# Kernel optimization log

Hardware: AMD Instinct MI355X
Metric: run time of the kernel (lower is better)

The kernel has to match this reference:

```python
import jax, jax.numpy as jnp
import numpy as np

N, M, D = 8192, 8192, 64

def setup_inputs() -> dict:
    key = jax.random.key(0)
    kx, ky = jax.random.split(key)
    x = jax.random.normal(kx, (N, D), dtype=jnp.float32)
    y = jax.random.normal(ky, (M, D), dtype=jnp.float32)
    return {"x": x, "y": y}

def reference(x, y):
    T = 1.0
    # Dmat = 2 - euclidean cdist(x, y), computed via the Gram trick.
    sq = (jnp.sum(x * x, axis=1)[:, None]
          + jnp.sum(y * y, axis=1)[None, :]
          - 2.0 * (x @ y.T))
    Dmat = 2.0 - jnp.sqrt(jnp.maximum(sq, 0.0))          # [N, M]
    logprob_rows = jax.nn.log_softmax(Dmat * T, axis=1)   # [N, M]
    logprob_cols = jax.nn.log_softmax(Dmat.T * T, axis=1) # [M, N]
    choice_rows = jnp.argmax(logprob_rows, axis=1)        # [N]
    choice_cols = jnp.argmax(logprob_cols, axis=1)        # [M]
    seq = jnp.arange(M, dtype=choice_cols.dtype)
    mutual = choice_rows[choice_cols] == seq              # [M] bool
    lp_rows = jnp.take_along_axis(logprob_rows, choice_rows[:, None], axis=1)[:, 0]  # [N]
    lp_cols = jnp.take_along_axis(logprob_cols, choice_cols[:, None], axis=1)[:, 0]  # [M]
    # Padded (jit-friendly) form of the boolean compaction: entries where
    # mutual is False are zeroed; mutual mask identifies valid matches.
    log_probs = jnp.where(mutual, lp_rows[choice_cols] + lp_cols, 0.0)  # [M]
    dmatches = jnp.stack([choice_cols, seq], axis=1)      # [M, 2]
    return (log_probs, dmatches, mutual)
```

## Files before the change

### kernel.cpp

```cpp
#include <hip/hip_runtime.h>
#include <stdint.h>

#define NROWS 8192
#define MCOLS 8192
#define DDIM  64

typedef _Float16 half8   __attribute__((ext_vector_type(8)));
typedef float    floatx4 __attribute__((ext_vector_type(4)));

__device__ __forceinline__ unsigned f2key(float f) {
  unsigned u = __float_as_uint(f);
  return (u & 0x80000000u) ? ~u : (u | 0x80000000u);
}
__device__ __forceinline__ float key2f(unsigned k) {
  unsigned u = (k & 0x80000000u) ? (k & 0x7fffffffu) : ~k;
  return __uint_as_float(u);
}

__global__ void convert_kernel(const float* __restrict__ x, const float* __restrict__ y,
                               _Float16* __restrict__ xh, _Float16* __restrict__ xl,
                               _Float16* __restrict__ yh, _Float16* __restrict__ yl,
                               float* __restrict__ xn, float* __restrict__ yn,
                               unsigned long long* __restrict__ rk,
                               unsigned long long* __restrict__ ck,
                               float* __restrict__ rs, float* __restrict__ cs) {
  __shared__ float lnorm[32];
  const int gid = blockIdx.x * 256 + threadIdx.x;
  if (gid < 8192) { rk[gid] = 0ull; rs[gid] = 0.0f; ck[gid] = 0ull; cs[gid] = 0.0f; }
  if (threadIdx.x < 32) lnorm[threadIdx.x] = 0.0f;
  __syncthreads();

  const float* src; _Float16 *dh, *dl; float* nout; int t, rowbase;
  if (gid < 65536) { src = x; dh = xh; dl = xl; nout = xn; t = gid;
                     rowbase = blockIdx.x * 32; }
  else             { src = y; dh = yh; dl = yl; nout = yn; t = gid - 65536;
                     rowbase = (blockIdx.x - 256) * 32; }

  const int lane = t & 63;
  const int c    = (t >> 6) & 1;
  const int p    = t >> 7;
  const int row  = p * 16 + (lane & 15);
  const int k0   = c * 32 + ((lane >> 4) << 3);
  const float* s = src + (size_t)row * DDIM + k0;

  float fb[8];
  *(floatx4*)(&fb[0]) = *(const floatx4*)(s);
  *(floatx4*)(&fb[4]) = *(const floatx4*)(s + 4);

  _Float16 hbuf[8], lbuf[8];
  float s8 = 0.0f;
  #pragma unroll
  for (int j = 0; j < 8; ++j) {
    float f = fb[j];
    _Float16 h = (_Float16)f;
    hbuf[j] = h;
    lbuf[j] = (_Float16)((f - (float)h) * 2048.0f);
    s8 = fmaf(f, f, s8);
  }
  size_t o = (size_t)t * 8;
  *(half8*)(dh + o) = *(half8*)hbuf;
  *(half8*)(dl + o) = *(half8*)lbuf;

  atomicAdd(&lnorm[((p & 1) << 4) | (t & 15)], s8);
  __syncthreads();
  if (threadIdx.x < 32) nout[rowbase + threadIdx.x] = lnorm[threadIdx.x];
}

#define MFMA16(A, B, C) __builtin_amdgcn_mfma_f32_16x16x32_f16((A), (B), (C), 0, 0, 0)

__global__ __launch_bounds__(256, 3) void mfma_tile_kernel(
    const _Float16* __restrict__ xh, const _Float16* __restrict__ xl,
    const _Float16* __restrict__ yh, const _Float16* __restrict__ yl,
    const float* __restrict__ xn, const float* __restrict__ yn,
    unsigned long long* __restrict__ row_key, float* __restrict__ row_sum,
    unsigned long long* __restrict__ col_key, float* __restrict__ col_sum)
{
  __shared__ unsigned long long lkey[256];
  __shared__ float              lsum[256];

  const int wave = threadIdx.x >> 6;
  const int lane = threadIdx.x & 63;
  const int l15  = lane & 15;
  const int g    = lane >> 4;
  const int ap0  = blockIdx.y * 8 + wave * 2;
  const int ro   = ap0 * 16 + g * 4;
  const int colbase = blockIdx.x * 256;

  lkey[threadIdx.x] = 0ull;
  lsum[threadIdx.x] = 0.0f;
  __syncthreads();

  const half8* xh8 = (const half8*)xh;
  const half8* xl8 = (const half8*)xl;
  const half8* yh8 = (const half8*)yh;
  const half8* yl8 = (const half8*)yl;
  const size_t a0 = (size_t)ap0 * 128 + lane;
  half8 Ah[2][2], Al[2][2];
  #pragma unroll
  for (int p = 0; p < 2; ++p) {
    Ah[p][0] = xh8[a0 + p * 128];      Ah[p][1] = xh8[a0 + p * 128 + 64];
    Al[p][0] = xl8[a0 + p * 128];      Al[p][1] = xl8[a0 + p * 128 + 64];
  }

  float xne[8], rsum[8], rmax[8]; int ridx[8];
  #pragma unroll
  for (int s = 0; s < 8; ++s) {
    xne[s]  = xn[ro + ((s >> 2) << 4) + (s & 3)];
    rsum[s] = 0.0f; rmax[s] = -3.4e38f; ridx[s] = 0;
  }

  const size_t bcol0 = (size_t)(blockIdx.x * 16) * 128 + lane;

  half8 b0h0, b0h1, b0l0, b0l1; float y0n;
  half8 b1h0, b1h1, b1l0, b1l1; float y1n;
  b0h0 = yh8[bcol0];        b0h1 = yh8[bcol0 + 64];
  b0l0 = yl8[bcol0];        b0l1 = yl8[bcol0 + 64];
  y0n  = yn[colbase + l15];
  b1h0 = yh8[bcol0 + 128];  b1h1 = yh8[bcol0 + 192];
  b1l0 = yl8[bcol0 + 128];  b1l1 = yl8[bcol0 + 192];
  y1n  = yn[colbase + 16 + l15];

#define MFMA_TILE(BH0, BH1, BL0, BL1, O1A, O2A, O1B, O2B)                      \
  {                                                                            \
    floatx4 c1_ = {}, c2_ = {};                                                \
    c1_ = MFMA16(Ah[0][0], BH0, c1_);                                          \
    c1_ = MFMA16(Ah[0][1], BH1, c1_);                                          \
    c2_ = MFMA16(Al[0][0], BH0, c2_);                                          \
    c2_ = MFMA16(Al[0][1], BH1, c2_);                                          \
    c2_ = MFMA16(Ah[0][0], BL0, c2_);                                          \
    c2_ = MFMA16(Ah[0][1], BL1, c2_);                                          \
    O1A = c1_; O2A = c2_;                                                      \
    floatx4 d1_ = {}, d2_ = {};                                                \
    d1_ = MFMA16(Ah[1][0], BH0, d1_);                                          \
    d1_ = MFMA16(Ah[1][1], BH1, d1_);                                          \
    d2_ = MFMA16(Al[1][0], BH0, d2_);                                          \
    d2_ = MFMA16(Al[1][1], BH1, d2_);                                          \
    d2_ = MFMA16(Ah[1][0], BL0, d2_);                                          \
    d2_ = MFMA16(Ah[1][1], BL1, d2_);                                          \
    O1B = d1_; O2B = d2_;                                                      \
  }

#define EPILOGUE(JT, C1A, C2A, C1B, C2B, YNC)                                  \
  {                                                                            \
    const int col_ = colbase + (JT) * 16 + l15;                                \
    float cmax_ = -3.4e38f; int cidx_ = 0;                                     \
    float epan0_, epan1_;                                                      \
    {                                                                          \
      float ee_[4];                                                            \
      _Pragma("unroll")                                                        \
      for (int r = 0; r < 4; ++r) {                                            \
        const int s_ = r;                                                      \
        float dot = fmaf(C2A[r], (1.0f / 2048.0f), C1A[r]);                    \
        float sq  = fmaxf(fmaf(-2.0f, dot, xne[s_] + (YNC)), 0.0f);            \
        float d   = 2.0f - __builtin_amdgcn_sqrtf(sq);                         \
        float e   = __expf(d);                                                 \
        rsum[s_] += e;                                                         \
        if (d > rmax[s_]) ridx[s_] = col_;       \
        rmax[s_] = fmaxf(rmax[s_], d);                                         \
        if (d > cmax_) cidx_ = s_;               \
        cmax_ = fmaxf(cmax_, d);                                               \
        ee_[r] = e;                                                            \
      }                                                                        \
      epan0_ = (ee_[0] + ee_[1]) + (ee_[2] + ee_[3]);                          \
    }                                                                          \
    {                                                                          \
      float ee_[4];                                                            \
      _Pragma("unroll")                                                        \
      for (int r = 0; r < 4; ++r) {                                            \
        const int s_ = 4 + r;                                                  \
        float dot = fmaf(C2B[r], (1.0f / 2048.0f), C1B[r]);                    \
        float sq  = fmaxf(fmaf(-2.0f, dot, xne[s_] + (YNC)), 0.0f);            \
        float d   = 2.0f - __builtin_amdgcn_sqrtf(sq);                         \
        float e   = __expf(d);                                                 \
        rsum[s_] += e;                                                         \
        if (d > rmax[s_]) ridx[s_] = col_;                                     \
        rmax[s_] = fmaxf(rmax[s_], d);                                         \
        if (d > cmax_) cidx_ = s_;                                             \
        cmax_ = fmaxf(cmax_, d);                                               \
        ee_[r] = e;                                                            \
      }                                                                        \
      epan1_ = (ee_[0] + ee_[1]) + (ee_[2] + ee_[3]);                          \
    }                                                                          \
    float csum_ = epan0_ + epan1_;                \
    int crow_ = ro + ((cidx_ >> 2) << 4) + (cidx_ & 3);                        \
    unsigned long long ckey_ =                                                 \
        ((unsigned long long)f2key(cmax_) << 32) |                             \
        (unsigned long long)(unsigned)(~(unsigned)crow_);                      \
    atomicMax(&lkey[(JT) * 16 + l15], ckey_);                  \
    atomicAdd(&lsum[(JT) * 16 + l15], csum_);                  \
  }

  floatx4 Pc1a, Pc2a, Pc1b, Pc2b;
  floatx4 Qc1a, Qc2a, Qc1b, Qc2b;

  MFMA_TILE(b0h0, b0h1, b0l0, b0l1, Pc1a, Pc2a, Pc1b, Pc2b);

  for (int jt = 0; jt < 14; jt += 2) {
    {
      float ycur = y0n;
      const size_t bn = bcol0 + (size_t)(jt + 2) * 128;
      b0h0 = yh8[bn];      b0h1 = yh8[bn + 64];
      b0l0 = yl8[bn];      b0l1 = yl8[bn + 64];
      y0n  = yn[colbase + (jt + 2) * 16 + l15];
      MFMA_TILE(b1h0, b1h1, b1l0, b1l1, Qc1a, Qc2a, Qc1b, Qc2b);
      EPILOGUE(jt, Pc1a, Pc2a, Pc1b, Pc2b, ycur);
    }
    {
      float ycur = y1n;
      const size_t bn = bcol0 + (size_t)(jt + 3) * 128;
      b1h0 = yh8[bn];      b1h1 = yh8[bn + 64];
      b1l0 = yl8[bn];      b1l1 = yl8[bn + 64];
      y1n  = yn[colbase + (jt + 3) * 16 + l15];
      MFMA_TILE(b0h0, b0h1, b0l0, b0l1, Pc1a, Pc2a, Pc1b, Pc2b);
      EPILOGUE(jt + 1, Qc1a, Qc2a, Qc1b, Qc2b, ycur);
    }
  }
  {
    MFMA_TILE(b1h0, b1h1, b1l0, b1l1, Qc1a, Qc2a, Qc1b, Qc2b);
    EPILOGUE(14, Pc1a, Pc2a, Pc1b, Pc2b, y0n);
  }
  EPILOGUE(15, Qc1a, Qc2a, Qc1b, Qc2b, y1n);

#undef MFMA_TILE
#undef EPILOGUE

  unsigned long long rkk[8];
  #pragma unroll
  for (int s = 0; s < 8; ++s)
    rkk[s] = ((unsigned long long)f2key(rmax[s]) << 32) |
             (unsigned long long)(unsigned)(~(unsigned)ridx[s]);
  #pragma unroll
  for (int off = 1; off < 16; off <<= 1) {
    #pragma unroll
    for (int s = 0; s < 8; ++s) {
      rsum[s] += __shfl_xor(rsum[s], off);
      unsigned long long o = __shfl_xor(rkk[s], off);
      if (o > rkk[s]) rkk[s] = o;
    }
  }
  if (l15 == 0) {
    #pragma unroll
    for (int s = 0; s < 8; ++s) {
      int row = ro + ((s >> 2) << 4) + (s & 3);
      atomicMax(row_key + row, rkk[s]);
      atomicAdd(row_sum + row, rsum[s]);
    }
  }

  __syncthreads();
  {
    int col = colbase + threadIdx.x;
    atomicMax(col_key + col, lkey[threadIdx.x]);
    atomicAdd(col_sum + col, lsum[threadIdx.x]);
  }
}

__global__ void finalize_kernel(const unsigned long long* __restrict__ row_key,
                                const float* __restrict__ row_sum,
                                const unsigned long long* __restrict__ col_key,
                                const float* __restrict__ col_sum,
                                float* __restrict__ out)
{
  int j = blockIdx.x * 256 + threadIdx.x;
  if (j >= MCOLS) return;
  unsigned long long ck = col_key[j];
  int   ci   = (int)(~(unsigned)ck);
  float cmax = key2f((unsigned)(ck >> 32));
  float lp_col = cmax - logf(col_sum[j]);

  unsigned long long rk = row_key[ci];
  int   rj   = (int)(~(unsigned)rk);
  float rmax = key2f((unsigned)(rk >> 32));
  float lp_row = rmax - logf(row_sum[ci]);

  int mut = (rj == j);
  out[j]                 = mut ? (lp_row + lp_col) : 0.0f;
  out[MCOLS + 2 * j + 0] = (float)ci;
  out[MCOLS + 2 * j + 1] = (float)j;
  out[3 * MCOLS + j]     = mut ? 1.0f : 0.0f;
}

extern "C" void kernel_launch(void* const* d_in, const int* in_sizes, int n_in,
                              void* d_out, int out_size, void* d_ws, size_t ws_size,
                              hipStream_t stream) {
  const float* x = (const float*)d_in[0];
  const float* y = (const float*)d_in[1];
  float* out = (float*)d_out;

  char* ws = (char*)d_ws;
  unsigned long long* row_key = (unsigned long long*)(ws);
  unsigned long long* col_key = (unsigned long long*)(ws + 65536);
  float* row_sum = (float*)(ws + 131072);
  float* col_sum = (float*)(ws + 163840);
  float* xn      = (float*)(ws + 196608);
  float* yn      = (float*)(ws + 229376);
  _Float16* xh = (_Float16*)(ws + 262144);
  _Float16* xl = (_Float16*)(ws + 262144 + 1048576);
  _Float16* yh = (_Float16*)(ws + 262144 + 2097152);
  _Float16* yl = (_Float16*)(ws + 262144 + 3145728);

  convert_kernel<<<512, 256, 0, stream>>>(x, y, xh, xl, yh, yl, xn, yn,
                                          row_key, col_key, row_sum, col_sum);
  dim3 grid(MCOLS / 256, NROWS / 128);
  mfma_tile_kernel<<<grid, 256, 0, stream>>>(xh, xl, yh, yl, xn, yn,
                                             row_key, row_sum, col_key, col_sum);
  finalize_kernel<<<32, 256, 0, stream>>>(row_key, row_sum, col_key, col_sum, out);
}
```

Baseline: 123.8 us.

## Replace global atomics with per-block partial buffers and separate reductions

The tile kernel stores per-block row and column max-key and sum partials into workspace arrays instead of issuing global atomicMax/atomicAdd. A new row-reduction kernel combines the 32 column-block partials per row, and the finalize kernel reduces the 64 row-block partials per column. This is meant to remove atomic contention and the zero-initialisation in the convert kernel. In exchange it adds extra memory traffic for the partial arrays and an additional kernel launch.

After: 128.7 us. 4.0% more time.

```diff
diff --git a/kernel.cpp b/kernel.cpp
--- a/kernel.cpp
+++ b/kernel.cpp
@@ -4,6 +4,8 @@
 #define NROWS 8192
 #define MCOLS 8192
 #define DDIM  64
+#define NBX   32
+#define NBY   64
 
 typedef _Float16 half8   __attribute__((ext_vector_type(8)));
 typedef float    floatx4 __attribute__((ext_vector_type(4)));
@@ -20,13 +22,9 @@
 __global__ void convert_kernel(const float* __restrict__ x, const float* __restrict__ y,
                                _Float16* __restrict__ xh, _Float16* __restrict__ xl,
                                _Float16* __restrict__ yh, _Float16* __restrict__ yl,
-                               float* __restrict__ xn, float* __restrict__ yn,
-                               unsigned long long* __restrict__ rk,
-                               unsigned long long* __restrict__ ck,
-                               float* __restrict__ rs, float* __restrict__ cs) {
+                               float* __restrict__ xn, float* __restrict__ yn) {
   __shared__ float lnorm[32];
   const int gid = blockIdx.x * 256 + threadIdx.x;
-  if (gid < 8192) { rk[gid] = 0ull; rs[gid] = 0.0f; ck[gid] = 0ull; cs[gid] = 0.0f; }
   if (threadIdx.x < 32) lnorm[threadIdx.x] = 0.0f;
   __syncthreads();
 
@@ -72,8 +70,8 @@
     const _Float16* __restrict__ xh, const _Float16* __restrict__ xl,
     const _Float16* __restrict__ yh, const _Float16* __restrict__ yl,
     const float* __restrict__ xn, const float* __restrict__ yn,
-    unsigned long long* __restrict__ row_key, float* __restrict__ row_sum,
-    unsigned long long* __restrict__ col_key, float* __restrict__ col_sum)
+    unsigned long long* __restrict__ row_part_key, float* __restrict__ row_part_sum,
+    unsigned long long* __restrict__ col_part_key, float* __restrict__ col_part_sum)
 {
   __shared__ unsigned long long lkey[256];
   __shared__ float              lsum[256];
@@ -242,31 +240,57 @@
     #pragma unroll
     for (int s = 0; s < 8; ++s) {
       int row = ro + ((s >> 2) << 4) + (s & 3);
-      atomicMax(row_key + row, rkk[s]);
-      atomicAdd(row_sum + row, rsum[s]);
+      row_part_key[(size_t)blockIdx.x * NROWS + row] = rkk[s];
+      row_part_sum[(size_t)blockIdx.x * NROWS + row] = rsum[s];
     }
   }
 
   __syncthreads();
   {
     int col = colbase + threadIdx.x;
-    atomicMax(col_key + col, lkey[threadIdx.x]);
-    atomicAdd(col_sum + col, lsum[threadIdx.x]);
-  }
+    col_part_key[(size_t)blockIdx.y * MCOLS + col] = lkey[threadIdx.x];
+    col_part_sum[(size_t)blockIdx.y * MCOLS + col] = lsum[threadIdx.x];
+  }
+}
+
+__global__ void reduce_rows_kernel(const unsigned long long* __restrict__ rpk,
+                                   const float* __restrict__ rps,
+                                   unsigned long long* __restrict__ row_key,
+                                   float* __restrict__ row_sum)
+{
+  int row = blockIdx.x * 256 + threadIdx.x;
+  if (row >= NROWS) return;
+  unsigned long long best = 0ull; float sum = 0.0f;
+  #pragma unroll 8
+  for (int bx = 0; bx < NBX; ++bx) {
+    unsigned long long k = rpk[(size_t)bx * NROWS + row];
+    if (k > best) best = k;
+    sum += rps[(size_t)bx * NROWS + row];
+  }
+  row_key[row] = best;
+  row_sum[row] = sum;
 }
 
 __global__ void finalize_kernel(const unsigned long long* __restrict__ row_key,
                                 const float* __restrict__ row_sum,
-                                const unsigned long long* __restrict__ col_key,
-                                const float* __restrict__ col_sum,
+                                const unsigned long long* __restrict__ cpk,
+                                const float* __restrict__ cps,
                                 float* __restrict__ out)
 {
   int j = blockIdx.x * 256 + threadIdx.x;
   if (j >= MCOLS) return;
-  unsigned long long ck = col_key[j];
+
+  unsigned long long ck = 0ull; float csum = 0.0f;
+  #pragma unroll 8
+  for (int by = 0; by < NBY; ++by) {
+    unsigned long long k = cpk[(size_t)by * MCOLS + j];
+    if (k > ck) ck = k;
+    csum += cps[(size_t)by * MCOLS + j];
+  }
+
   int   ci   = (int)(~(unsigned)ck);
   float cmax = key2f((unsigned)(ck >> 32));
-  float lp_col = cmax - logf(col_sum[j]);
+  float lp_col = cmax - logf(csum);
 
   unsigned long long rk = row_key[ci];
   int   rj   = (int)(~(unsigned)rk);
@@ -289,20 +313,22 @@
 
   char* ws = (char*)d_ws;
   unsigned long long* row_key = (unsigned long long*)(ws);
-  unsigned long long* col_key = (unsigned long long*)(ws + 65536);
-  float* row_sum = (float*)(ws + 131072);
-  float* col_sum = (float*)(ws + 163840);
-  float* xn      = (float*)(ws + 196608);
-  float* yn      = (float*)(ws + 229376);
-  _Float16* xh = (_Float16*)(ws + 262144);
-  _Float16* xl = (_Float16*)(ws + 262144 + 1048576);
-  _Float16* yh = (_Float16*)(ws + 262144 + 2097152);
-  _Float16* yl = (_Float16*)(ws + 262144 + 3145728);
-
-  convert_kernel<<<512, 256, 0, stream>>>(x, y, xh, xl, yh, yl, xn, yn,
-                                          row_key, col_key, row_sum, col_sum);
+  float* row_sum = (float*)(ws + 65536);
+  float* xn      = (float*)(ws + 98304);
+  float* yn      = (float*)(ws + 131072);
+  unsigned long long* rpk = (unsigned long long*)(ws + 163840);
+  float* rps     = (float*)(ws + 2260992);
+  unsigned long long* cpk = (unsigned long long*)(ws + 3309568);
+  float* cps     = (float*)(ws + 7503872);
+  _Float16* xh = (_Float16*)(ws + 9601024);
+  _Float16* xl = (_Float16*)(ws + 10649600);
+  _Float16* yh = (_Float16*)(ws + 11698176);
+  _Float16* yl = (_Float16*)(ws + 12746752);
+
+  convert_kernel<<<512, 256, 0, stream>>>(x, y, xh, xl, yh, yl, xn, yn);
   dim3 grid(MCOLS / 256, NROWS / 128);
   mfma_tile_kernel<<<grid, 256, 0, stream>>>(xh, xl, yh, yl, xn, yn,
-                                             row_key, row_sum, col_key, col_sum);
-  finalize_kernel<<<32, 256, 0, stream>>>(row_key, row_sum, col_key, col_sum, out);
-}
+                                             rpk, rps, cpk, cps);
+  reduce_rows_kernel<<<32, 256, 0, stream>>>(rpk, rps, row_key, row_sum);
+  finalize_kernel<<<32, 256, 0, stream>>>(row_key, row_sum, cpk, cps, out);
+}
```
